# Kernel optimization log

Hardware: AMD Instinct MI355X
Metric: run time of the kernel (lower is better)

Reference implementation:

```python
import jax, jax.numpy as jnp
import numpy as np

B, T, I, H, SEQLEN = 16384, 60, 32, 128, 30


def setup_inputs() -> dict:
    key = jax.random.key(0)
    ks = jax.random.split(key, 8)
    s_ih = 1.0 / np.sqrt(H)
    return {
        "x": jax.random.normal(ks[0], (B, T, I), dtype=jnp.float32),
        "h": jax.random.normal(ks[1], (1, B, H), dtype=jnp.float32),
        # GRU params (PyTorch layout: gates [r, z, n] stacked along dim 0)
        "W_ih": jax.random.uniform(ks[2], (3 * H, I), minval=-s_ih, maxval=s_ih, dtype=jnp.float32),
        "W_hh": jax.random.uniform(ks[3], (3 * H, H), minval=-s_ih, maxval=s_ih, dtype=jnp.float32),
        "b_ih": jax.random.uniform(ks[4], (3 * H,), minval=-s_ih, maxval=s_ih, dtype=jnp.float32),
        "b_hh": jax.random.uniform(ks[5], (3 * H,), minval=-s_ih, maxval=s_ih, dtype=jnp.float32),
        # output projection: hidden -> n_inputs
        "W_out": jax.random.uniform(ks[6], (I, H), minval=-s_ih, maxval=s_ih, dtype=jnp.float32),
        "b_out": jax.random.uniform(ks[7], (I,), minval=-s_ih, maxval=s_ih, dtype=jnp.float32),
    }


def _gru_cell(x_t, h, W_ih, W_hh, b_ih, b_hh):
    # x_t: [B, I], h: [B, H]
    gi = x_t @ W_ih.T + b_ih          # [B, 3H]
    gh = h @ W_hh.T + b_hh            # [B, 3H]
    i_r, i_z, i_n = jnp.split(gi, 3, axis=-1)
    h_r, h_z, h_n = jnp.split(gh, 3, axis=-1)
    r = jax.nn.sigmoid(i_r + h_r)
    z = jax.nn.sigmoid(i_z + h_z)
    n = jnp.tanh(i_n + r * h_n)
    return (1.0 - z) * n + z * h


def reference(x, h, W_ih, W_hh, b_ih, b_hh, W_out, b_out):
    xout = x[:, SEQLEN:, :]            # [B, steps, I]
    steps = xout.shape[1]
    h0 = h[0]                          # single layer, unidirectional -> [B, H]
    x0 = xout[:, 0, :]                 # [B, I]

    def step(carry, _):
        x_t, h_t = carry
        h_new = _gru_cell(x_t, h_t, W_ih, W_hh, b_ih, b_hh)
        y = h_new @ W_out.T + b_out    # [B, I], fed back as next input
        return (y, h_new), y

    _, ys = jax.lax.scan(step, (x0, h0), None, length=steps)  # ys: [steps, B, I]
    return jnp.transpose(ys, (1, 0, 2))                        # [B, steps, I]
```

## Files before the change

kernel.cpp:

```cpp
#include <hip/hip_runtime.h>


#define NB    16384
#define TT    60
#define II    32
#define HH    128
#define NSTEP 30
#define SEQ0  30
#define BM    32
#define HBS   144
#define XBS   40

#define WS_WSTAR 0
#define WS_BSTAR (384 * 128)

typedef __attribute__((ext_vector_type(8))) short bf16x8;
typedef __attribute__((ext_vector_type(4))) float f32x4;

#define MFMA(a, b, c) __builtin_amdgcn_mfma_f32_16x16x32_bf16((a), (b), (c), 0, 0, 0)

#define LDS_BARRIER() do {                                        \
    asm volatile("s_waitcnt lgkmcnt(0)\n\ts_barrier" ::: "memory"); \
    __builtin_amdgcn_sched_barrier(0);                            \
} while (0)

__device__ __forceinline__ short f2bf(float x) {
    unsigned u = __float_as_uint(x);
    u += 0x7FFFu + ((u >> 16) & 1u);
    return (short)(u >> 16);
}
__device__ __forceinline__ bf16x8 ldw8(const float* p) {
    float4 a = *(const float4*)p;
    float4 b = *(const float4*)(p + 4);
    bf16x8 f;
    f[0] = f2bf(a.x); f[1] = f2bf(a.y); f[2] = f2bf(a.z); f[3] = f2bf(a.w);
    f[4] = f2bf(b.x); f[5] = f2bf(b.y); f[6] = f2bf(b.z); f[7] = f2bf(b.w);
    return f;
}
__device__ __forceinline__ float sigm(float a) {
    return __builtin_amdgcn_rcpf(1.0f + __expf(-a));
}
__device__ __forceinline__ float tanh_(float a) {
    return 1.0f - 2.0f * __builtin_amdgcn_rcpf(1.0f + __expf(2.0f * a));
}

__global__ void fold_kernel(const float* __restrict__ Wih,
                            const float* __restrict__ Whh,
                            const float* __restrict__ bih,
                            const float* __restrict__ bhh,
                            const float* __restrict__ Wout,
                            const float* __restrict__ bout,
                            float* __restrict__ ws)
{
    const int jg = blockIdx.x;
    const int k  = threadIdx.x;
    const int gate = jg >> 7;
    float acc  = (gate < 2) ? Whh[(size_t)jg * HH + k] : 0.0f;
    float bacc = 0.0f;
    #pragma unroll 8
    for (int i = 0; i < II; ++i) {
        const float w = Wih[(size_t)jg * II + i];
        acc  += w * Wout[(size_t)i * HH + k];
        bacc += w * bout[i];
    }
    ws[WS_WSTAR + (size_t)jg * HH + k] = acc;
    if (k == 0)
        ws[WS_BSTAR + jg] = bih[jg] + ((gate < 2) ? bhh[jg] : 0.0f) + bacc;
}

__global__ __launch_bounds__(512, 2)
void gru_mfma_kernel(const float* __restrict__ x,
                     const float* __restrict__ h0,
                     const float* __restrict__ Wih,
                     const float* __restrict__ Whh,
                     const float* __restrict__ bih,
                     const float* __restrict__ bhh,
                     const float* __restrict__ Wout,
                     const float* __restrict__ bout,
                     const float* __restrict__ ws,
                     float* __restrict__ out)
{
    __shared__ short shb[2][BM * HBS];
    __shared__ short sxb[BM * XBS];
    __shared__ short sWo[2 * 4 * 64 * 8];

    const int tid    = threadIdx.x;
    const int lane   = tid & 63;
    const int wave   = __builtin_amdgcn_readfirstlane(tid >> 6);
    const int n16    = lane & 15;
    const int quad   = lane >> 4;
    const int rowblk = blockIdx.x * BM;
    const int j      = wave * 16 + n16;

    bf16x8 Bnh[4];
    float  b_nh;
    {
        const float* wn = Whh + (size_t)(2 * HH + j) * HH;
        #pragma unroll
        for (int kt = 0; kt < 4; ++kt)
            Bnh[kt] = ldw8(wn + kt * 32 + quad * 8);
        b_nh = bhh[2 * HH + j];
    }
    const int rowtile = wave >> 1;
    const int coltile = wave & 1;
    float b_o = 0.0f;
    if (wave < 2) {
        #pragma unroll
        for (int kt = 0; kt < 4; ++kt) {
            bf16x8 t = ldw8(Wout + (size_t)(wave * 16 + n16) * HH + kt * 32 + quad * 8);
            *(bf16x8*)&sWo[((wave * 4 + kt) * 64 + lane) * 8] = t;
        }
    }
    if (wave < 4) b_o = bout[coltile * 16 + n16];

    float hst[2][4];
    #pragma unroll
    for (int mt = 0; mt < 2; ++mt)
        #pragma unroll
        for (int reg = 0; reg < 4; ++reg)
            hst[mt][reg] = h0[(size_t)(rowblk + mt * 16 + quad * 4 + reg) * HH + j];

    {
        const int r  = tid >> 4;
        const int c0 = (tid & 15) * 8;
        *(bf16x8*)&shb[0][r * HBS + c0] = ldw8(h0 + (size_t)(rowblk + r) * HH + c0);
    }
    if (tid < 128) {
        const int r  = tid >> 2;
        const int c0 = (tid & 3) * 8;
        *(bf16x8*)&sxb[r * XBS + c0] = ldw8(x + ((size_t)(rowblk + r) * TT + SEQ0) * II + c0);
    }
    __syncthreads();

    {
        bf16x8 Br0[4], Bz0[4], Bxr, Bxz, Bxn;
        const float* wr = Whh + (size_t)j * HH;
        const float* wz = Whh + (size_t)(HH + j) * HH;
        #pragma unroll
        for (int kt = 0; kt < 4; ++kt) {
            Br0[kt] = ldw8(wr + kt * 32 + quad * 8);
            Bz0[kt] = ldw8(wz + kt * 32 + quad * 8);
        }
        Bxr = ldw8(Wih + (size_t)j * II + quad * 8);
        Bxz = ldw8(Wih + (size_t)(HH + j) * II + quad * 8);
        Bxn = ldw8(Wih + (size_t)(2 * HH + j) * II + quad * 8);
        const float b_r0 = bih[j] + bhh[j];
        const float b_z0 = bih[HH + j] + bhh[HH + j];
        const float b_n0 = bih[2 * HH + j];

        #pragma unroll
        for (int mt = 0; mt < 2; ++mt) {
            f32x4 ar  = (f32x4){b_r0, b_r0, b_r0, b_r0};
            f32x4 az  = (f32x4){b_z0, b_z0, b_z0, b_z0};
            f32x4 anh = (f32x4){b_nh, b_nh, b_nh, b_nh};
            f32x4 anx = (f32x4){b_n0, b_n0, b_n0, b_n0};
            #pragma unroll
            for (int kt = 0; kt < 4; ++kt) {
                bf16x8 A = *(const bf16x8*)&shb[0][(mt * 16 + n16) * HBS + kt * 32 + quad * 8];
                ar  = MFMA(A, Br0[kt], ar);
                az  = MFMA(A, Bz0[kt], az);
                anh = MFMA(A, Bnh[kt], anh);
            }
            {
                bf16x8 Ax = *(const bf16x8*)&sxb[(mt * 16 + n16) * XBS + quad * 8];
                ar  = MFMA(Ax, Bxr, ar);
                az  = MFMA(Ax, Bxz, az);
                anx = MFMA(Ax, Bxn, anx);
            }
            #pragma unroll
            for (int reg = 0; reg < 4; ++reg) {
                const float r = sigm(ar[reg]);
                const float z = sigm(az[reg]);
                const float n = tanh_(anx[reg] + r * anh[reg]);
                const float hnew = n + z * (hst[mt][reg] - n);
                hst[mt][reg] = hnew;
                shb[1][(mt * 16 + quad * 4 + reg) * HBS + j] = f2bf(hnew);
            }
        }
    }

    bf16x8 Brs[4], Bzs[4], Bni[4];
    float  b_rs, b_zs, b_ni;
    {
        const float* pr = ws + WS_WSTAR + (size_t)j * HH;
        const float* pz = ws + WS_WSTAR + (size_t)(HH + j) * HH;
        const float* pn = ws + WS_WSTAR + (size_t)(2 * HH + j) * HH;
        #pragma unroll
        for (int kt = 0; kt < 4; ++kt) {
            Brs[kt] = ldw8(pr + kt * 32 + quad * 8);
            Bzs[kt] = ldw8(pz + kt * 32 + quad * 8);
            Bni[kt] = ldw8(pn + kt * 32 + quad * 8);
        }
        b_rs = ws[WS_BSTAR + j];
        b_zs = ws[WS_BSTAR + HH + j];
        b_ni = ws[WS_BSTAR + 2 * HH + j];
    }

    __syncthreads();

    int p = 0;
    for (int s = 0; s < NSTEP; ++s) {
        const int q = 1 - p;

        if (wave < 4) {
            f32x4 yo = (f32x4){b_o, b_o, b_o, b_o};
            #pragma unroll
            for (int kt = 0; kt < 4; ++kt) {
                bf16x8 A2  = *(const bf16x8*)&shb[q][(rowtile * 16 + n16) * HBS + kt * 32 + quad * 8];
                bf16x8 Bof = *(const bf16x8*)&sWo[((coltile * 4 + kt) * 64 + lane) * 8];
                yo = MFMA(A2, Bof, yo);
            }
            #pragma unroll
            for (int reg = 0; reg < 4; ++reg) {
                const int r_l = rowtile * 16 + quad * 4 + reg;
                out[(size_t)(rowblk + r_l) * (NSTEP * II) + s * II + coltile * 16 + n16] = yo[reg];
            }
        }

        if (s == NSTEP - 1) break;

        #pragma unroll
        for (int mt = 0; mt < 2; ++mt) {
            f32x4 ar  = (f32x4){b_rs, b_rs, b_rs, b_rs};
            f32x4 az  = (f32x4){b_zs, b_zs, b_zs, b_zs};
            f32x4 anh = (f32x4){b_nh, b_nh, b_nh, b_nh};
            f32x4 ani = (f32x4){b_ni, b_ni, b_ni, b_ni};
            #pragma unroll
            for (int kt = 0; kt < 4; ++kt) {
                bf16x8 A = *(const bf16x8*)&shb[q][(mt * 16 + n16) * HBS + kt * 32 + quad * 8];
                ar  = MFMA(A, Brs[kt], ar);
                az  = MFMA(A, Bzs[kt], az);
                anh = MFMA(A, Bnh[kt], anh);
                ani = MFMA(A, Bni[kt], ani);
            }
            #pragma unroll
            for (int reg = 0; reg < 4; ++reg) {
                const float r = sigm(ar[reg]);
                const float z = sigm(az[reg]);
                const float n = tanh_(ani[reg] + r * anh[reg]);
                const float hnew = n + z * (hst[mt][reg] - n);
                hst[mt][reg] = hnew;
                shb[p][(mt * 16 + quad * 4 + reg) * HBS + j] = f2bf(hnew);
            }
        }

        p = q;
        LDS_BARRIER();
    }
}

extern "C" void kernel_launch(void* const* d_in, const int* in_sizes, int n_in,
                              void* d_out, int out_size, void* d_ws, size_t ws_size,
                              hipStream_t stream) {
    (void)in_sizes; (void)n_in; (void)out_size; (void)ws_size;
    const float* x    = (const float*)d_in[0];
    const float* h0   = (const float*)d_in[1];
    const float* Wih  = (const float*)d_in[2];
    const float* Whh  = (const float*)d_in[3];
    const float* bih  = (const float*)d_in[4];
    const float* bhh  = (const float*)d_in[5];
    const float* Wout = (const float*)d_in[6];
    const float* bout = (const float*)d_in[7];
    float* out = (float*)d_out;
    float* ws  = (float*)d_ws;

    fold_kernel<<<dim3(384), dim3(128), 0, stream>>>(Wih, Whh, bih, bhh,
                                                     Wout, bout, ws);
    dim3 grid(NB / BM);
    dim3 block(512);
    gru_mfma_kernel<<<grid, block, 0, stream>>>(x, h0, Wih, Whh, bih, bhh,
                                                Wout, bout, ws, out);
}
```

Measured before the change: 281.8 us.

## Halve block to 4 waves with two column tiles each; prescale gates for exp2

Each block now runs 256 threads (4 waves) instead of 512, and each wave computes two 16-column hidden tiles. This reuses every A-fragment LDS load across both tiles and keeps twice the weight fragments in registers. Gate weights and biases are prescaled by -log2(e) or 2*log2(e), so sigmoid and tanh evaluate with a raw exp2 and no extra multiply. The cost is higher register pressure per thread and half as many waves per block to hide MFMA and LDS latency.

```diff
diff --git a/kernel.cpp b/kernel.cpp
--- a/kernel.cpp
+++ b/kernel.cpp
@@ -14,15 +14,25 @@
 #define WS_WSTAR 0
 #define WS_BSTAR (384 * 128)
 
+#define S_RZ (-1.4426950408889634f)
+#define S_N  ( 2.8853900817779268f)
+
 typedef __attribute__((ext_vector_type(8))) short bf16x8;
 typedef __attribute__((ext_vector_type(4))) float f32x4;
 
 #define MFMA(a, b, c) __builtin_amdgcn_mfma_f32_16x16x32_bf16((a), (b), (c), 0, 0, 0)
 
-#define LDS_BARRIER() do {                                        \
+#define LDS_BARRIER() do {                                          \
     asm volatile("s_waitcnt lgkmcnt(0)\n\ts_barrier" ::: "memory"); \
-    __builtin_amdgcn_sched_barrier(0);                            \
+    __builtin_amdgcn_sched_barrier(0);                              \
 } while (0)
+
+#if __has_builtin(__builtin_amdgcn_exp2f)
+#define EXP2(x) __builtin_amdgcn_exp2f(x)
+#else
+#define EXP2(x) exp2f(x)
+#endif
+#define RCP(x) __builtin_amdgcn_rcpf(x)
 
 __device__ __forceinline__ short f2bf(float x) {
     unsigned u = __float_as_uint(x);
@@ -37,11 +47,19 @@
     f[4] = f2bf(b.x); f[5] = f2bf(b.y); f[6] = f2bf(b.z); f[7] = f2bf(b.w);
     return f;
 }
-__device__ __forceinline__ float sigm(float a) {
-    return __builtin_amdgcn_rcpf(1.0f + __expf(-a));
-}
-__device__ __forceinline__ float tanh_(float a) {
-    return 1.0f - 2.0f * __builtin_amdgcn_rcpf(1.0f + __expf(2.0f * a));
+__device__ __forceinline__ bf16x8 ldw8s(const float* p, float s) {
+    float4 a = *(const float4*)p;
+    float4 b = *(const float4*)(p + 4);
+    bf16x8 f;
+    f[0] = f2bf(a.x * s); f[1] = f2bf(a.y * s); f[2] = f2bf(a.z * s); f[3] = f2bf(a.w * s);
+    f[4] = f2bf(b.x * s); f[5] = f2bf(b.y * s); f[6] = f2bf(b.z * s); f[7] = f2bf(b.w * s);
+    return f;
+}
+__device__ __forceinline__ float sigm2(float ap) {
+    return RCP(1.0f + EXP2(ap));
+}
+__device__ __forceinline__ float tanh2(float tp) {
+    return fmaf(-2.0f, RCP(1.0f + EXP2(tp)), 1.0f);
 }
 
 __global__ void fold_kernel(const float* __restrict__ Wih,
@@ -55,6 +73,7 @@
     const int jg = blockIdx.x;
     const int k  = threadIdx.x;
     const int gate = jg >> 7;
+    const float sc = (gate < 2) ? S_RZ : S_N;
     float acc  = (gate < 2) ? Whh[(size_t)jg * HH + k] : 0.0f;
     float bacc = 0.0f;
     #pragma unroll 8
@@ -63,12 +82,12 @@
         acc  += w * Wout[(size_t)i * HH + k];
         bacc += w * bout[i];
     }
-    ws[WS_WSTAR + (size_t)jg * HH + k] = acc;
+    ws[WS_WSTAR + (size_t)jg * HH + k] = acc * sc;
     if (k == 0)
-        ws[WS_BSTAR + jg] = bih[jg] + ((gate < 2) ? bhh[jg] : 0.0f) + bacc;
-}
-
-__global__ __launch_bounds__(512, 2)
+        ws[WS_BSTAR + jg] = (bih[jg] + ((gate < 2) ? bhh[jg] : 0.0f) + bacc) * sc;
+}
+
+__global__ __launch_bounds__(256, 2)
 void gru_mfma_kernel(const float* __restrict__ x,
                      const float* __restrict__ h0,
                      const float* __restrict__ Wih,
@@ -90,20 +109,20 @@
     const int n16    = lane & 15;
     const int quad   = lane >> 4;
     const int rowblk = blockIdx.x * BM;
-    const int j      = wave * 16 + n16;
-
-    bf16x8 Bnh[4];
-    float  b_nh;
-    {
-        const float* wn = Whh + (size_t)(2 * HH + j) * HH;
+
+    bf16x8 Bnh[2][4];
+    float  b_nh[2];
+    #pragma unroll
+    for (int ct = 0; ct < 2; ++ct) {
+        const int jc = wave * 32 + ct * 16 + n16;
+        const float* wn = Whh + (size_t)(2 * HH + jc) * HH;
         #pragma unroll
         for (int kt = 0; kt < 4; ++kt)
-            Bnh[kt] = ldw8(wn + kt * 32 + quad * 8);
-        b_nh = bhh[2 * HH + j];
-    }
-    const int rowtile = wave >> 1;
-    const int coltile = wave & 1;
-    float b_o = 0.0f;
+            Bnh[ct][kt] = ldw8s(wn + kt * 32 + quad * 8, S_N);
+        b_nh[ct] = bhh[2 * HH + jc] * S_N;
+    }
+    const int mt2 = wave >> 1;
+    const int ct2 = wave & 1;
     if (wave < 2) {
         #pragma unroll
         for (int kt = 0; kt < 4; ++kt) {
@@ -111,19 +130,24 @@
             *(bf16x8*)&sWo[((wave * 4 + kt) * 64 + lane) * 8] = t;
         }
     }
-    if (wave < 4) b_o = bout[coltile * 16 + n16];
-
-    float hst[2][4];
+    const float b_o = bout[ct2 * 16 + n16];
+
+    float hst[2][2][4];
     #pragma unroll
     for (int mt = 0; mt < 2; ++mt)
         #pragma unroll
-        for (int reg = 0; reg < 4; ++reg)
-            hst[mt][reg] = h0[(size_t)(rowblk + mt * 16 + quad * 4 + reg) * HH + j];
+        for (int ct = 0; ct < 2; ++ct)
+            #pragma unroll
+            for (int reg = 0; reg < 4; ++reg)
+                hst[mt][ct][reg] =
+                    h0[(size_t)(rowblk + mt * 16 + quad * 4 + reg) * HH + wave * 32 + ct * 16 + n16];
 
     {
-        const int r  = tid >> 4;
-        const int c0 = (tid & 15) * 8;
-        *(bf16x8*)&shb[0][r * HBS + c0] = ldw8(h0 + (size_t)(rowblk + r) * HH + c0);
+        const int r  = tid >> 3;
+        const int c0 = (tid & 7) * 16;
+        const float* src = h0 + (size_t)(rowblk + r) * HH + c0;
+        *(bf16x8*)&shb[0][r * HBS + c0]     = ldw8(src);
+        *(bf16x8*)&shb[0][r * HBS + c0 + 8] = ldw8(src + 8);
     }
     if (tid < 128) {
         const int r  = tid >> 2;
@@ -132,34 +156,36 @@
     }
     __syncthreads();
 
-    {
-        bf16x8 Br0[4], Bz0[4], Bxr, Bxz, Bxn;
-        const float* wr = Whh + (size_t)j * HH;
-        const float* wz = Whh + (size_t)(HH + j) * HH;
+    #pragma unroll
+    for (int ct = 0; ct < 2; ++ct) {
+        const int jc = wave * 32 + ct * 16 + n16;
+        bf16x8 Br0[4], Bz0[4];
+        const float* wr = Whh + (size_t)jc * HH;
+        const float* wz = Whh + (size_t)(HH + jc) * HH;
         #pragma unroll
         for (int kt = 0; kt < 4; ++kt) {
-            Br0[kt] = ldw8(wr + kt * 32 + quad * 8);
-            Bz0[kt] = ldw8(wz + kt * 32 + quad * 8);
-        }
-        Bxr = ldw8(Wih + (size_t)j * II + quad * 8);
-        Bxz = ldw8(Wih + (size_t)(HH + j) * II + quad * 8);
-        Bxn = ldw8(Wih + (size_t)(2 * HH + j) * II + quad * 8);
-        const float b_r0 = bih[j] + bhh[j];
-        const float b_z0 = bih[HH + j] + bhh[HH + j];
-        const float b_n0 = bih[2 * HH + j];
+            Br0[kt] = ldw8s(wr + kt * 32 + quad * 8, S_RZ);
+            Bz0[kt] = ldw8s(wz + kt * 32 + quad * 8, S_RZ);
+        }
+        bf16x8 Bxr = ldw8s(Wih + (size_t)jc * II + quad * 8, S_RZ);
+        bf16x8 Bxz = ldw8s(Wih + (size_t)(HH + jc) * II + quad * 8, S_RZ);
+        bf16x8 Bxn = ldw8s(Wih + (size_t)(2 * HH + jc) * II + quad * 8, S_N);
+        const float b_r0 = (bih[jc] + bhh[jc]) * S_RZ;
+        const float b_z0 = (bih[HH + jc] + bhh[HH + jc]) * S_RZ;
+        const float b_n0 = bih[2 * HH + jc] * S_N;
 
         #pragma unroll
         for (int mt = 0; mt < 2; ++mt) {
             f32x4 ar  = (f32x4){b_r0, b_r0, b_r0, b_r0};
             f32x4 az  = (f32x4){b_z0, b_z0, b_z0, b_z0};
-            f32x4 anh = (f32x4){b_nh, b_nh, b_nh, b_nh};
+            f32x4 anh = (f32x4){b_nh[ct], b_nh[ct], b_nh[ct], b_nh[ct]};
             f32x4 anx = (f32x4){b_n0, b_n0, b_n0, b_n0};
             #pragma unroll
             for (int kt = 0; kt < 4; ++kt) {
                 bf16x8 A = *(const bf16x8*)&shb[0][(mt * 16 + n16) * HBS + kt * 32 + quad * 8];
                 ar  = MFMA(A, Br0[kt], ar);
                 az  = MFMA(A, Bz0[kt], az);
-                anh = MFMA(A, Bnh[kt], anh);
+                anh = MFMA(A, Bnh[ct][kt], anh);
             }
             {
                 bf16x8 Ax = *(const bf16x8*)&sxb[(mt * 16 + n16) * XBS + quad * 8];
@@ -169,31 +195,33 @@
             }
             #pragma unroll
             for (int reg = 0; reg < 4; ++reg) {
-                const float r = sigm(ar[reg]);
-                const float z = sigm(az[reg]);
-                const float n = tanh_(anx[reg] + r * anh[reg]);
-                const float hnew = n + z * (hst[mt][reg] - n);
-                hst[mt][reg] = hnew;
-                shb[1][(mt * 16 + quad * 4 + reg) * HBS + j] = f2bf(hnew);
-            }
-        }
-    }
-
-    bf16x8 Brs[4], Bzs[4], Bni[4];
-    float  b_rs, b_zs, b_ni;
-    {
-        const float* pr = ws + WS_WSTAR + (size_t)j * HH;
-        const float* pz = ws + WS_WSTAR + (size_t)(HH + j) * HH;
-        const float* pn = ws + WS_WSTAR + (size_t)(2 * HH + j) * HH;
+                const float r = sigm2(ar[reg]);
+                const float z = sigm2(az[reg]);
+                const float n = tanh2(anx[reg] + r * anh[reg]);
+                const float hnew = n + z * (hst[mt][ct][reg] - n);
+                hst[mt][ct][reg] = hnew;
+                shb[1][(mt * 16 + quad * 4 + reg) * HBS + wave * 32 + ct * 16 + n16] = f2bf(hnew);
+            }
+        }
+    }
+
+    bf16x8 Brs[2][4], Bzs[2][4], Bni[2][4];
+    float  b_rs[2], b_zs[2], b_ni[2];
+    #pragma unroll
+    for (int ct = 0; ct < 2; ++ct) {
+        const int jc = wave * 32 + ct * 16 + n16;
+        const float* pr = ws + WS_WSTAR + (size_t)jc * HH;
+        const float* pz = ws + WS_WSTAR + (size_t)(HH + jc) * HH;
+        const float* pn = ws + WS_WSTAR + (size_t)(2 * HH + jc) * HH;
         #pragma unroll
         for (int kt = 0; kt < 4; ++kt) {
-            Brs[kt] = ldw8(pr + kt * 32 + quad * 8);
-            Bzs[kt] = ldw8(pz + kt * 32 + quad * 8);
-            Bni[kt] = ldw8(pn + kt * 32 + quad * 8);
-        }
-        b_rs = ws[WS_BSTAR + j];
-        b_zs = ws[WS_BSTAR + HH + j];
-        b_ni = ws[WS_BSTAR + 2 * HH + j];
+            Brs[ct][kt] = ldw8(pr + kt * 32 + quad * 8);
+            Bzs[ct][kt] = ldw8(pz + kt * 32 + quad * 8);
+            Bni[ct][kt] = ldw8(pn + kt * 32 + quad * 8);
+        }
+        b_rs[ct] = ws[WS_BSTAR + jc];
+        b_zs[ct] = ws[WS_BSTAR + HH + jc];
+        b_ni[ct] = ws[WS_BSTAR + 2 * HH + jc];
     }
 
     __syncthreads();
@@ -202,18 +230,18 @@
     for (int s = 0; s < NSTEP; ++s) {
         const int q = 1 - p;
 
-        if (wave < 4) {
+        {
             f32x4 yo = (f32x4){b_o, b_o, b_o, b_o};
             #pragma unroll
             for (int kt = 0; kt < 4; ++kt) {
-                bf16x8 A2  = *(const bf16x8*)&shb[q][(rowtile * 16 + n16) * HBS + kt * 32 + quad * 8];
-                bf16x8 Bof = *(const bf16x8*)&sWo[((coltile * 4 + kt) * 64 + lane) * 8];
+                bf16x8 A2  = *(const bf16x8*)&shb[q][(mt2 * 16 + n16) * HBS + kt * 32 + quad * 8];
+                bf16x8 Bof = *(const bf16x8*)&sWo[((ct2 * 4 + kt) * 64 + lane) * 8];
                 yo = MFMA(A2, Bof, yo);
             }
             #pragma unroll
             for (int reg = 0; reg < 4; ++reg) {
-                const int r_l = rowtile * 16 + quad * 4 + reg;
-                out[(size_t)(rowblk + r_l) * (NSTEP * II) + s * II + coltile * 16 + n16] = yo[reg];
+                const int r_l = mt2 * 16 + quad * 4 + reg;
+                out[(size_t)(rowblk + r_l) * (NSTEP * II) + s * II + ct2 * 16 + n16] = yo[reg];
             }
         }
 
@@ -221,26 +249,33 @@
 
         #pragma unroll
         for (int mt = 0; mt < 2; ++mt) {
-            f32x4 ar  = (f32x4){b_rs, b_rs, b_rs, b_rs};
-            f32x4 az  = (f32x4){b_zs, b_zs, b_zs, b_zs};
-            f32x4 anh = (f32x4){b_nh, b_nh, b_nh, b_nh};
-            f32x4 ani = (f32x4){b_ni, b_ni, b_ni, b_ni};
-            #pragma unroll
-            for (int kt = 0; kt < 4; ++kt) {
-                bf16x8 A = *(const bf16x8*)&shb[q][(mt * 16 + n16) * HBS + kt * 32 + quad * 8];
-                ar  = MFMA(A, Brs[kt], ar);
-                az  = MFMA(A, Bzs[kt], az);
-                anh = MFMA(A, Bnh[kt], anh);
-                ani = MFMA(A, Bni[kt], ani);
-            }
-            #pragma unroll
-            for (int reg = 0; reg < 4; ++reg) {
-                const float r = sigm(ar[reg]);
-                const float z = sigm(az[reg]);
-                const float n = tanh_(ani[reg] + r * anh[reg]);
-                const float hnew = n + z * (hst[mt][reg] - n);
-                hst[mt][reg] = hnew;
-                shb[p][(mt * 16 + quad * 4 + reg) * HBS + j] = f2bf(hnew);
+            bf16x8 A[4];
+            #pragma unroll
+            for (int kt = 0; kt < 4; ++kt)
+                A[kt] = *(const bf16x8*)&shb[q][(mt * 16 + n16) * HBS + kt * 32 + quad * 8];
+
+            #pragma unroll
+            for (int ct = 0; ct < 2; ++ct) {
+                f32x4 ar  = (f32x4){b_rs[ct], b_rs[ct], b_rs[ct], b_rs[ct]};
+                f32x4 az  = (f32x4){b_zs[ct], b_zs[ct], b_zs[ct], b_zs[ct]};
+                f32x4 anh = (f32x4){b_nh[ct], b_nh[ct], b_nh[ct], b_nh[ct]};
+                f32x4 ani = (f32x4){b_ni[ct], b_ni[ct], b_ni[ct], b_ni[ct]};
+                #pragma unroll
+                for (int kt = 0; kt < 4; ++kt) {
+                    ar  = MFMA(A[kt], Brs[ct][kt], ar);
+                    az  = MFMA(A[kt], Bzs[ct][kt], az);
+                    anh = MFMA(A[kt], Bnh[ct][kt], anh);
+                    ani = MFMA(A[kt], Bni[ct][kt], ani);
+                }
+                #pragma unroll
+                for (int reg = 0; reg < 4; ++reg) {
+                    const float r = sigm2(ar[reg]);
+                    const float z = sigm2(az[reg]);
+                    const float n = tanh2(ani[reg] + r * anh[reg]);
+                    const float hnew = n + z * (hst[mt][ct][reg] - n);
+                    hst[mt][ct][reg] = hnew;
+                    shb[p][(mt * 16 + quad * 4 + reg) * HBS + wave * 32 + ct * 16 + n16] = f2bf(hnew);
+                }
             }
         }
 
@@ -267,7 +302,7 @@
     fold_kernel<<<dim3(384), dim3(128), 0, stream>>>(Wih, Whh, bih, bhh,
                                                      Wout, bout, ws);
     dim3 grid(NB / BM);
-    dim3 block(512);
+    dim3 block(256);
     gru_mfma_kernel<<<grid, block, 0, stream>>>(x, h0, Wih, Whh, bih, bhh,
                                                 Wout, bout, ws, out);
 }
```

Result: no change. 287.3 us (+2.0%).

## Double GRU row tile to 64, swizzle LDS hidden state, fold exp2 scaling

Applied to the files above, without the earlier changes.

Each block now processes 64 batch rows instead of 32. Launch bounds drop to one block per CU, and all 8 waves compute the output projection with Wout held in registers instead of LDS. The hidden-state LDS buffer switches from padded rows to an XOR-swizzled layout to avoid bank conflicts. The log2e and 2·log2e factors are folded into the weights and biases so sigmoid and tanh use exp2 directly. Writes use packed bf16 conversion, and the time loop is unrolled by two so buffer indices are static. The trade-off is higher register pressure, lower occupancy and half as many blocks.

```diff
diff --git a/kernel.cpp b/kernel.cpp
--- a/kernel.cpp
+++ b/kernel.cpp
@@ -7,27 +7,39 @@
 #define HH    128
 #define NSTEP 30
 #define SEQ0  30
-#define BM    32
-#define HBS   144
+#define BM    64
 #define XBS   40
+#define ROWB  256
+#define BUFB  (BM * ROWB)
 
 #define WS_WSTAR 0
 #define WS_BSTAR (384 * 128)
 
+#define S_RZ (-1.4426950408889634f)
+#define S_N  ( 2.8853900817779268f)
+
 typedef __attribute__((ext_vector_type(8))) short bf16x8;
 typedef __attribute__((ext_vector_type(4))) float f32x4;
 
 #define MFMA(a, b, c) __builtin_amdgcn_mfma_f32_16x16x32_bf16((a), (b), (c), 0, 0, 0)
 
-#define LDS_BARRIER() do {                                        \
+#define LDS_BARRIER() do {                                          \
     asm volatile("s_waitcnt lgkmcnt(0)\n\ts_barrier" ::: "memory"); \
-    __builtin_amdgcn_sched_barrier(0);                            \
+    __builtin_amdgcn_sched_barrier(0);                              \
 } while (0)
+
+#define EXP2(x) __builtin_amdgcn_exp2f(x)
+#define RCP(x)  __builtin_amdgcn_rcpf(x)
 
 __device__ __forceinline__ short f2bf(float x) {
     unsigned u = __float_as_uint(x);
     u += 0x7FFFu + ((u >> 16) & 1u);
     return (short)(u >> 16);
+}
+__device__ __forceinline__ unsigned cvt_pk_bf16(float lo, float hi) {
+    unsigned r;
+    asm("v_cvt_pk_bf16_f32 %0, %1, %2" : "=v"(r) : "v"(lo), "v"(hi));
+    return r;
 }
 __device__ __forceinline__ bf16x8 ldw8(const float* p) {
     float4 a = *(const float4*)p;
@@ -37,11 +49,17 @@
     f[4] = f2bf(b.x); f[5] = f2bf(b.y); f[6] = f2bf(b.z); f[7] = f2bf(b.w);
     return f;
 }
-__device__ __forceinline__ float sigm(float a) {
-    return __builtin_amdgcn_rcpf(1.0f + __expf(-a));
-}
-__device__ __forceinline__ float tanh_(float a) {
-    return 1.0f - 2.0f * __builtin_amdgcn_rcpf(1.0f + __expf(2.0f * a));
+__device__ __forceinline__ bf16x8 ldw8s(const float* p, float s) {
+    float4 a = *(const float4*)p;
+    float4 b = *(const float4*)(p + 4);
+    bf16x8 f;
+    f[0] = f2bf(a.x * s); f[1] = f2bf(a.y * s); f[2] = f2bf(a.z * s); f[3] = f2bf(a.w * s);
+    f[4] = f2bf(b.x * s); f[5] = f2bf(b.y * s); f[6] = f2bf(b.z * s); f[7] = f2bf(b.w * s);
+    return f;
+}
+__device__ __forceinline__ float sigm2(float ap) { return RCP(1.0f + EXP2(ap)); }
+__device__ __forceinline__ float tanh2(float tp) {
+    return fmaf(-2.0f, RCP(1.0f + EXP2(tp)), 1.0f);
 }
 
 __global__ void fold_kernel(const float* __restrict__ Wih,
@@ -55,6 +73,7 @@
     const int jg = blockIdx.x;
     const int k  = threadIdx.x;
     const int gate = jg >> 7;
+    const float sc = (gate < 2) ? S_RZ : S_N;
     float acc  = (gate < 2) ? Whh[(size_t)jg * HH + k] : 0.0f;
     float bacc = 0.0f;
     #pragma unroll 8
@@ -63,12 +82,12 @@
         acc  += w * Wout[(size_t)i * HH + k];
         bacc += w * bout[i];
     }
-    ws[WS_WSTAR + (size_t)jg * HH + k] = acc;
+    ws[WS_WSTAR + (size_t)jg * HH + k] = acc * sc;
     if (k == 0)
-        ws[WS_BSTAR + jg] = bih[jg] + ((gate < 2) ? bhh[jg] : 0.0f) + bacc;
-}
-
-__global__ __launch_bounds__(512, 2)
+        ws[WS_BSTAR + jg] = (bih[jg] + ((gate < 2) ? bhh[jg] : 0.0f) + bacc) * sc;
+}
+
+__global__ __launch_bounds__(512, 1)
 void gru_mfma_kernel(const float* __restrict__ x,
                      const float* __restrict__ h0,
                      const float* __restrict__ Wih,
@@ -80,9 +99,9 @@
                      const float* __restrict__ ws,
                      float* __restrict__ out)
 {
-    __shared__ short shb[2][BM * HBS];
+    __shared__ short shb[2][BM * 128];
     __shared__ short sxb[BM * XBS];
-    __shared__ short sWo[2 * 4 * 64 * 8];
+    char* shbb = (char*)shb;
 
     const int tid    = threadIdx.x;
     const int lane   = tid & 63;
@@ -92,40 +111,60 @@
     const int rowblk = blockIdx.x * BM;
     const int j      = wave * 16 + n16;
 
+    int rb[4];
+    #pragma unroll
+    for (int kt = 0; kt < 4; ++kt)
+        rb[kt] = n16 * 256 + ((kt * 64 + quad * 16) ^ (n16 << 4));
+    int wb[4];
+    #pragma unroll
+    for (int rg = 0; rg < 4; ++rg)
+        wb[rg] = quad * 1024 + ((2 * j) ^ (quad << 6) ^ (rg << 4));
+
     bf16x8 Bnh[4];
     float  b_nh;
     {
         const float* wn = Whh + (size_t)(2 * HH + j) * HH;
         #pragma unroll
         for (int kt = 0; kt < 4; ++kt)
-            Bnh[kt] = ldw8(wn + kt * 32 + quad * 8);
-        b_nh = bhh[2 * HH + j];
+            Bnh[kt] = ldw8s(wn + kt * 32 + quad * 8, S_N);
+        b_nh = bhh[2 * HH + j] * S_N;
     }
     const int rowtile = wave >> 1;
     const int coltile = wave & 1;
-    float b_o = 0.0f;
-    if (wave < 2) {
-        #pragma unroll
-        for (int kt = 0; kt < 4; ++kt) {
-            bf16x8 t = ldw8(Wout + (size_t)(wave * 16 + n16) * HH + kt * 32 + quad * 8);
-            *(bf16x8*)&sWo[((wave * 4 + kt) * 64 + lane) * 8] = t;
-        }
-    }
-    if (wave < 4) b_o = bout[coltile * 16 + n16];
-
-    float hst[2][4];
+    bf16x8 Bo[4];
+    float  b_o;
+    {
+        const int i = coltile * 16 + n16;
+        #pragma unroll
+        for (int kt = 0; kt < 4; ++kt)
+            Bo[kt] = ldw8(Wout + (size_t)i * HH + kt * 32 + quad * 8);
+        b_o = bout[i];
+    }
+
+    float hst[4][4];
     #pragma unroll
-    for (int mt = 0; mt < 2; ++mt)
+    for (int mt = 0; mt < 4; ++mt)
         #pragma unroll
         for (int reg = 0; reg < 4; ++reg)
             hst[mt][reg] = h0[(size_t)(rowblk + mt * 16 + quad * 4 + reg) * HH + j];
 
-    {
-        const int r  = tid >> 4;
-        const int c0 = (tid & 15) * 8;
-        *(bf16x8*)&shb[0][r * HBS + c0] = ldw8(h0 + (size_t)(rowblk + r) * HH + c0);
-    }
-    if (tid < 128) {
+    float* yp0;
+    float* yp1;
+    {
+        const int r0 = rowblk + rowtile * 16 + quad * 4;
+        yp0 = out + (size_t)r0 * (NSTEP * II) + coltile * 16 + n16;
+        yp1 = yp0 + 2 * (size_t)(NSTEP * II);
+    }
+
+    {
+        const int r  = tid >> 3;
+        const int cb = (tid & 7) * 32;
+        const int sw = (r & 15) << 4;
+        const float* src = h0 + (size_t)(rowblk + r) * HH + (tid & 7) * 16;
+        *(bf16x8*)(shbb + r * ROWB + (cb ^ sw))        = ldw8(src);
+        *(bf16x8*)(shbb + r * ROWB + ((cb + 16) ^ sw)) = ldw8(src + 8);
+    }
+    if (tid < 256) {
         const int r  = tid >> 2;
         const int c0 = (tid & 3) * 8;
         *(bf16x8*)&sxb[r * XBS + c0] = ldw8(x + ((size_t)(rowblk + r) * TT + SEQ0) * II + c0);
@@ -138,25 +177,25 @@
         const float* wz = Whh + (size_t)(HH + j) * HH;
         #pragma unroll
         for (int kt = 0; kt < 4; ++kt) {
-            Br0[kt] = ldw8(wr + kt * 32 + quad * 8);
-            Bz0[kt] = ldw8(wz + kt * 32 + quad * 8);
-        }
-        Bxr = ldw8(Wih + (size_t)j * II + quad * 8);
-        Bxz = ldw8(Wih + (size_t)(HH + j) * II + quad * 8);
-        Bxn = ldw8(Wih + (size_t)(2 * HH + j) * II + quad * 8);
-        const float b_r0 = bih[j] + bhh[j];
-        const float b_z0 = bih[HH + j] + bhh[HH + j];
-        const float b_n0 = bih[2 * HH + j];
-
-        #pragma unroll
-        for (int mt = 0; mt < 2; ++mt) {
+            Br0[kt] = ldw8s(wr + kt * 32 + quad * 8, S_RZ);
+            Bz0[kt] = ldw8s(wz + kt * 32 + quad * 8, S_RZ);
+        }
+        Bxr = ldw8s(Wih + (size_t)j * II + quad * 8, S_RZ);
+        Bxz = ldw8s(Wih + (size_t)(HH + j) * II + quad * 8, S_RZ);
+        Bxn = ldw8s(Wih + (size_t)(2 * HH + j) * II + quad * 8, S_N);
+        const float b_r0 = (bih[j] + bhh[j]) * S_RZ;
+        const float b_z0 = (bih[HH + j] + bhh[HH + j]) * S_RZ;
+        const float b_n0 = bih[2 * HH + j] * S_N;
+
+        #pragma unroll
+        for (int mt = 0; mt < 4; ++mt) {
             f32x4 ar  = (f32x4){b_r0, b_r0, b_r0, b_r0};
             f32x4 az  = (f32x4){b_z0, b_z0, b_z0, b_z0};
             f32x4 anh = (f32x4){b_nh, b_nh, b_nh, b_nh};
             f32x4 anx = (f32x4){b_n0, b_n0, b_n0, b_n0};
             #pragma unroll
             for (int kt = 0; kt < 4; ++kt) {
-                bf16x8 A = *(const bf16x8*)&shb[0][(mt * 16 + n16) * HBS + kt * 32 + quad * 8];
+                bf16x8 A = *(const bf16x8*)(shbb + rb[kt] + mt * 4096);
                 ar  = MFMA(A, Br0[kt], ar);
                 az  = MFMA(A, Bz0[kt], az);
                 anh = MFMA(A, Bnh[kt], anh);
@@ -167,15 +206,22 @@
                 az  = MFMA(Ax, Bxz, az);
                 anx = MFMA(Ax, Bxn, anx);
             }
+            float hn[4];
             #pragma unroll
             for (int reg = 0; reg < 4; ++reg) {
-                const float r = sigm(ar[reg]);
-                const float z = sigm(az[reg]);
-                const float n = tanh_(anx[reg] + r * anh[reg]);
+                const float r = sigm2(ar[reg]);
+                const float z = sigm2(az[reg]);
+                const float n = tanh2(anx[reg] + r * anh[reg]);
                 const float hnew = n + z * (hst[mt][reg] - n);
                 hst[mt][reg] = hnew;
-                shb[1][(mt * 16 + quad * 4 + reg) * HBS + j] = f2bf(hnew);
-            }
+                hn[reg] = hnew;
+            }
+            const unsigned pk01 = cvt_pk_bf16(hn[0], hn[1]);
+            const unsigned pk23 = cvt_pk_bf16(hn[2], hn[3]);
+            *(short*)(shbb + BUFB + wb[0] + mt * 4096)       = (short)pk01;
+            *(short*)(shbb + BUFB + wb[1] + mt * 4096 + 256) = (short)(pk01 >> 16);
+            *(short*)(shbb + BUFB + wb[2] + mt * 4096 + 512) = (short)pk23;
+            *(short*)(shbb + BUFB + wb[3] + mt * 4096 + 768) = (short)(pk23 >> 16);
         }
     }
 
@@ -198,55 +244,66 @@
 
     __syncthreads();
 
-    int p = 0;
-    for (int s = 0; s < NSTEP; ++s) {
-        const int q = 1 - p;
-
-        if (wave < 4) {
+    auto body = [&](int s, int qb, bool last) {
+        (void)s;
+        const int rdoff = qb * BUFB;
+        {
             f32x4 yo = (f32x4){b_o, b_o, b_o, b_o};
             #pragma unroll
             for (int kt = 0; kt < 4; ++kt) {
-                bf16x8 A2  = *(const bf16x8*)&shb[q][(rowtile * 16 + n16) * HBS + kt * 32 + quad * 8];
-                bf16x8 Bof = *(const bf16x8*)&sWo[((coltile * 4 + kt) * 64 + lane) * 8];
-                yo = MFMA(A2, Bof, yo);
-            }
-            #pragma unroll
-            for (int reg = 0; reg < 4; ++reg) {
-                const int r_l = rowtile * 16 + quad * 4 + reg;
-                out[(size_t)(rowblk + r_l) * (NSTEP * II) + s * II + coltile * 16 + n16] = yo[reg];
-            }
-        }
-
-        if (s == NSTEP - 1) break;
-
-        #pragma unroll
-        for (int mt = 0; mt < 2; ++mt) {
+                bf16x8 A2 = *(const bf16x8*)(shbb + rdoff + rb[kt] + rowtile * 4096);
+                yo = MFMA(A2, Bo[kt], yo);
+            }
+            yp0[0]         = yo[0];
+            yp0[NSTEP*II]  = yo[1];
+            yp1[0]         = yo[2];
+            yp1[NSTEP*II]  = yo[3];
+            yp0 += II;
+            yp1 += II;
+        }
+        if (last) return;
+
+        const int wroff = (qb ^ 1) * BUFB;
+        #pragma unroll
+        for (int mt = 0; mt < 4; ++mt) {
             f32x4 ar  = (f32x4){b_rs, b_rs, b_rs, b_rs};
             f32x4 az  = (f32x4){b_zs, b_zs, b_zs, b_zs};
             f32x4 anh = (f32x4){b_nh, b_nh, b_nh, b_nh};
             f32x4 ani = (f32x4){b_ni, b_ni, b_ni, b_ni};
             #pragma unroll
             for (int kt = 0; kt < 4; ++kt) {
-                bf16x8 A = *(const bf16x8*)&shb[q][(mt * 16 + n16) * HBS + kt * 32 + quad * 8];
+                bf16x8 A = *(const bf16x8*)(shbb + rdoff + rb[kt] + mt * 4096);
                 ar  = MFMA(A, Brs[kt], ar);
                 az  = MFMA(A, Bzs[kt], az);
                 anh = MFMA(A, Bnh[kt], anh);
                 ani = MFMA(A, Bni[kt], ani);
             }
+            float hn[4];
             #pragma unroll
             for (int reg = 0; reg < 4; ++reg) {
-                const float r = sigm(ar[reg]);
-                const float z = sigm(az[reg]);
-                const float n = tanh_(ani[reg] + r * anh[reg]);
+                const float r = sigm2(ar[reg]);
+                const float z = sigm2(az[reg]);
+                const float n = tanh2(ani[reg] + r * anh[reg]);
                 const float hnew = n + z * (hst[mt][reg] - n);
                 hst[mt][reg] = hnew;
-                shb[p][(mt * 16 + quad * 4 + reg) * HBS + j] = f2bf(hnew);
-            }
-        }
-
-        p = q;
+                hn[reg] = hnew;
+            }
+            const unsigned pk01 = cvt_pk_bf16(hn[0], hn[1]);
+            const unsigned pk23 = cvt_pk_bf16(hn[2], hn[3]);
+            *(short*)(shbb + wroff + wb[0] + mt * 4096)       = (short)pk01;
+            *(short*)(shbb + wroff + wb[1] + mt * 4096 + 256) = (short)(pk01 >> 16);
+            *(short*)(shbb + wroff + wb[2] + mt * 4096 + 512) = (short)pk23;
+            *(short*)(shbb + wroff + wb[3] + mt * 4096 + 768) = (short)(pk23 >> 16);
+        }
         LDS_BARRIER();
-    }
+    };
+
+    for (int s2 = 0; s2 < NSTEP - 2; s2 += 2) {
+        body(s2,     1, false);
+        body(s2 + 1, 0, false);
+    }
+    body(NSTEP - 2, 1, false);
+    body(NSTEP - 1, 0, true);
 }
 
 extern "C" void kernel_launch(void* const* d_in, const int* in_sizes, int n_in,
```

Result: faster. 256.8 us (-8.9%).
